# Performance work log

Hardware: AMD Instinct MI355X
Metric: run time of the kernel (lower is better)

Reference implementation:

```python
import jax, jax.numpy as jnp
import numpy as np

N, D, K, H = 16384, 2048, 8, 8
HD = D // H
LN_EPS = 1e-5


def setup_inputs() -> dict:
    key = jax.random.key(0)
    ks = jax.random.split(key, 12)
    w = lambda k: jax.random.normal(k, (D, D), dtype=jnp.float32) * 0.02
    return {
        "hidden": jax.random.normal(ks[0], (N, D), dtype=jnp.float32),
        "memory": jax.random.normal(ks[1], (K, D), dtype=jnp.float32) * 0.02,
        "w_read_q": w(ks[2]), "w_read_k": w(ks[3]), "w_read_v": w(ks[4]),
        "w_read_out": w(ks[5]),
        "w_write_q": w(ks[6]), "w_write_k": w(ks[7]), "w_write_v": w(ks[8]),
        "ln_gamma": jnp.ones((D,), dtype=jnp.float32),
        "ln_beta": jnp.zeros((D,), dtype=jnp.float32),
        "gate": jnp.full((1,), -3.0, dtype=jnp.float32),
        "write_gate": jnp.full((1,), -2.0, dtype=jnp.float32),
    }


def _layernorm(x, gamma, beta):
    mu = jnp.mean(x, axis=-1, keepdims=True)
    var = jnp.mean(jnp.square(x - mu), axis=-1, keepdims=True)
    return (x - mu) * jax.lax.rsqrt(var + LN_EPS) * gamma + beta


def reference(hidden, memory, w_read_q, w_read_k, w_read_v, w_read_out,
              w_write_q, w_write_k, w_write_v, ln_gamma, ln_beta, gate, write_gate):
    # --- read: cross-attention from tokens (queries) to memory slots (keys/values) ---
    q = (hidden @ w_read_q.T).reshape(N, H, HD)   # [N,H,hd]
    k = (memory @ w_read_k.T).reshape(K, H, HD)   # [K,H,hd]
    v = (memory @ w_read_v.T).reshape(K, H, HD)
    scores = jnp.einsum("nhd,khd->hnk", q, k) / np.sqrt(HD).astype(np.float32)
    attn = jax.nn.softmax(scores, axis=-1)        # [H,N,K]
    read_out = jnp.einsum("hnk,khd->nhd", attn, v).reshape(N, D)
    cross_info = _layernorm(read_out, ln_gamma, ln_beta) @ w_read_out.T
    g = jax.nn.sigmoid(gate[0])
    result = hidden + g * cross_info              # [N,D]
    # --- write: memory slots (queries) attend over all tokens, gated EMA update ---
    wq = memory @ w_write_q.T                     # [K,D]
    wk = hidden @ w_write_k.T                     # [N,D]
    wv = hidden @ w_write_v.T                     # [N,D]
    wattn = jax.nn.softmax(wq @ wk.T / np.sqrt(D).astype(np.float32), axis=-1)  # [K,N]
    new_info = wattn @ wv                         # [K,D]
    wg = jax.nn.sigmoid(write_gate[0])
    new_memory = (1.0 - wg) * memory + wg * new_info
    return result, new_memory
```

## Files before the change

kernel.cpp:

```cpp
#include <hip/hip_runtime.h>
#include <hip/hip_bf16.h>
#include <stdint.h>

static constexpr int N_ = 16384;
static constexpr int D_ = 2048;
static constexpr float SCALE_R = 1.0f / 16.0f;
static constexpr float SCALE_W = 0.02209708691207961f;

typedef __bf16 bf16x8 __attribute__((ext_vector_type(8)));
typedef float f32x4 __attribute__((ext_vector_type(4)));

__device__ __forceinline__ unsigned short f2bf(float f) {
  unsigned int u = __float_as_uint(f);
  unsigned int r = (u + 0x7fff + ((u >> 16) & 1)) >> 16;
  return (unsigned short)r;
}

__device__ __forceinline__ void lds_load16(void* lds, const void* g) {
  __builtin_amdgcn_global_load_lds(
      (const __attribute__((address_space(1))) uint32_t*)(uintptr_t)g,
      (__attribute__((address_space(3))) uint32_t*)(uint32_t)(uintptr_t)lds,
      16, 0, 0);
}

__global__ __launch_bounds__(256) void k_kvwq(
    const float* __restrict__ mem, const float* __restrict__ wrk,
    const float* __restrict__ wrv, const float* __restrict__ wwq,
    float* __restrict__ kbuf, float* __restrict__ vbuf, float* __restrict__ wqbuf) {
  int gw = (blockIdx.x * 256 + threadIdx.x) >> 6;
  int lane = threadIdx.x & 63;
  int which = gw >> 11;
  int j = gw & 2047;
  const float* W = which == 0 ? wrk : (which == 1 ? wrv : wwq);
  float* O = which == 0 ? kbuf : (which == 1 ? vbuf : wqbuf);
  const f32x4* Wrow = (const f32x4*)(W + (size_t)j * D_);
  const f32x4* M4 = (const f32x4*)mem;
  float acc[8];
#pragma unroll
  for (int kk = 0; kk < 8; ++kk) acc[kk] = 0.f;
#pragma unroll
  for (int t = 0; t < 8; ++t) {
    f32x4 w4 = Wrow[lane + 64 * t];
#pragma unroll
    for (int kk = 0; kk < 8; ++kk) {
      f32x4 m4 = M4[kk * 512 + lane + 64 * t];
      acc[kk] += w4[0] * m4[0] + w4[1] * m4[1] + w4[2] * m4[2] + w4[3] * m4[3];
    }
  }
#pragma unroll
  for (int off = 1; off < 64; off <<= 1)
#pragma unroll
    for (int kk = 0; kk < 8; ++kk) acc[kk] += __shfl_xor(acc[kk], off, 64);
  if (lane == 0) {
#pragma unroll
    for (int kk = 0; kk < 8; ++kk) O[kk * D_ + j] = acc[kk];
  }
}

__global__ __launch_bounds__(256) void k_pr(
    const float* __restrict__ wrq, const float* __restrict__ wwk,
    const float* __restrict__ kbuf, const float* __restrict__ wqbuf,
    float* __restrict__ PRT) {
  int b = blockIdx.x;
  int tid = threadIdx.x;
  int half = b & 1;
  int sub = (b >> 1) & 7;
  int ic = (b >> 4) & 7;
  int i = ic * 256 + tid;
  bool isP = b < 128;
  const float* W = isP ? wrq : wwk;
  const float* V = isP ? kbuf : wqbuf;
  float scale = isP ? SCALE_R : SCALE_W;
  int rowbase = isP ? sub * 8 : 64;
  float acc[8];
#pragma unroll
  for (int kk = 0; kk < 8; ++kk) acc[kk] = 0.f;
  for (int jj = half * 128; jj < half * 128 + 128; ++jj) {
    int j = sub * 256 + jj;
    float wv = W[(size_t)j * D_ + i];
#pragma unroll
    for (int kk = 0; kk < 8; ++kk) acc[kk] += wv * V[kk * D_ + j];
  }
#pragma unroll
  for (int kk = 0; kk < 8; ++kk)
    atomicAdd(&PRT[(rowbase + kk) * D_ + i], acc[kk] * scale);
}

__global__ __launch_bounds__(256) void k_prep(const float* __restrict__ wro,
                                              const float* __restrict__ gamma,
                                              const float* __restrict__ beta,
                                              unsigned short* __restrict__ wp,
                                              float* __restrict__ c1, float* __restrict__ c2) {
  __shared__ float red1[4], red2[4];
  int j = blockIdx.x;
  int tid = threadIdx.x;
  int d = tid * 8;
  const float* src = wro + (size_t)j * D_ + d;
  f32x4 a = *(const f32x4*)src, b = *(const f32x4*)(src + 4);
  f32x4 g0 = *(const f32x4*)(gamma + d), g1 = *(const f32x4*)(gamma + d + 4);
  f32x4 b0 = *(const f32x4*)(beta + d), b1 = *(const f32x4*)(beta + d + 4);
  ushort4 o0, o1;
  o0.x = f2bf(a[0] * g0[0]); o0.y = f2bf(a[1] * g0[1]);
  o0.z = f2bf(a[2] * g0[2]); o0.w = f2bf(a[3] * g0[3]);
  o1.x = f2bf(b[0] * g1[0]); o1.y = f2bf(b[1] * g1[1]);
  o1.z = f2bf(b[2] * g1[2]); o1.w = f2bf(b[3] * g1[3]);
  unsigned short* dst = wp + (size_t)j * D_ + d;
  *(ushort4*)dst = o0;
  *(ushort4*)(dst + 4) = o1;
  float s1 = a[0] * g0[0] + a[1] * g0[1] + a[2] * g0[2] + a[3] * g0[3] +
             b[0] * g1[0] + b[1] * g1[1] + b[2] * g1[2] + b[3] * g1[3];
  float s2 = a[0] * b0[0] + a[1] * b0[1] + a[2] * b0[2] + a[3] * b0[3] +
             b[0] * b1[0] + b[1] * b1[1] + b[2] * b1[2] + b[3] * b1[3];
#pragma unroll
  for (int off = 1; off < 64; off <<= 1) {
    s1 += __shfl_xor(s1, off, 64);
    s2 += __shfl_xor(s2, off, 64);
  }
  int wave = tid >> 6, lane = tid & 63;
  if (lane == 0) { red1[wave] = s1; red2[wave] = s2; }
  __syncthreads();
  if (tid == 0) {
    c1[j] = red1[0] + red1[1] + red1[2] + red1[3];
    c2[j] = red2[0] + red2[1] + red2[2] + red2[3];
  }
}

__global__ __launch_bounds__(256) void k_main(
    const float* __restrict__ hidden, const float* __restrict__ PRT,
    const float* __restrict__ vbuf,
    unsigned short* __restrict__ Xhat, float* __restrict__ mu_out,
    float* __restrict__ rstd_out,
    float* __restrict__ upart, float* __restrict__ Zpart) {
  __shared__ unsigned short Ah[2][64 * 64];
  __shared__ unsigned short Bh[2][80 * 64];
  __shared__ unsigned short attnL[64 * 64];
  __shared__ float e8lds[64][8];
  const int tid = threadIdx.x;
  const int row0 = blockIdx.x * 64;
  const int wave = tid >> 6, lane = tid & 63;
  const int fl = lane & 15, fk = lane >> 4;
  const int ar = tid >> 2, acg = tid & 3;

  f32x4 sA0[4], sB0[5], sA1[4], sB1[5];

  auto loadAB = [&](f32x4* a, f32x4* b, int t) {
    const float* srcA = hidden + (size_t)(row0 + ar) * D_ + t * 64 + acg * 16;
#pragma unroll
    for (int q = 0; q < 4; ++q) a[q] = *(const f32x4*)(srcA + q * 4);
#pragma unroll
    for (int p = 0; p < 5; ++p) {
      int e = p * 256 + tid;
      int rB = e >> 4, c4 = e & 15;
      b[p] = *(const f32x4*)(PRT + (size_t)rB * D_ + t * 64 + c4 * 4);
    }
  };
  auto writeAB = [&](int buf, f32x4* a, f32x4* b) {
#pragma unroll
    for (int hh = 0; hh < 2; ++hh) {
      f32x4 x = a[hh * 2], y = a[hh * 2 + 1];
      ushort4 o0 = {f2bf(x[0]), f2bf(x[1]), f2bf(x[2]), f2bf(x[3])};
      ushort4 o1 = {f2bf(y[0]), f2bf(y[1]), f2bf(y[2]), f2bf(y[3])};
      int idx = (ar * 64 + acg * 16 + hh * 8) ^ ((ar & 7) << 3);
      *(ushort4*)&Ah[buf][idx] = o0;
      *(ushort4*)&Ah[buf][idx + 4] = o1;
    }
#pragma unroll
    for (int p = 0; p < 5; ++p) {
      int e = p * 256 + tid;
      int rB = e >> 4, c4 = e & 15;
      ushort4 o = {f2bf(b[p][0]), f2bf(b[p][1]), f2bf(b[p][2]), f2bf(b[p][3])};
      int idx = (rB * 64 + c4 * 4) ^ ((rB & 7) << 3);
      *(ushort4*)&Bh[buf][idx] = o;
    }
  };

  f32x4 acc[5];
#pragma unroll
  for (int n = 0; n < 5; ++n) acc[n] = (f32x4){0.f, 0.f, 0.f, 0.f};

  auto compute = [&](int buf) {
#pragma unroll
    for (int kk = 0; kk < 2; ++kk) {
      int klo = kk * 32 + fk * 8;
      bf16x8 af = *(const bf16x8*)&Ah[buf][((wave * 16 + fl) * 64 + klo) ^ ((fl & 7) << 3)];
#pragma unroll
      for (int n = 0; n < 5; ++n) {
        bf16x8 bf = *(const bf16x8*)&Bh[buf][((n * 16 + fl) * 64 + klo) ^ ((fl & 7) << 3)];
        acc[n] = __builtin_amdgcn_mfma_f32_16x16x32_bf16(af, bf, acc[n], 0, 0, 0);
      }
    }
  };

  loadAB(sA0, sB0, 0);
  loadAB(sA1, sB1, 1);
  for (int t = 0; t < 32; t += 2) {
    writeAB(0, sA0, sB0);
    if (t + 2 < 32) loadAB(sA0, sB0, t + 2);
    __syncthreads();
    compute(0);
    writeAB(1, sA1, sB1);
    if (t + 3 < 32) loadAB(sA1, sB1, t + 3);
    __syncthreads();
    compute(1);
  }

#pragma unroll
  for (int r = 0; r < 4; ++r) {
    int rowl = wave * 16 + fk * 4 + r;
#pragma unroll
    for (int n = 0; n < 4; ++n) {
      float sv = acc[n][r];
      float m = sv;
      m = fmaxf(m, __shfl_xor(m, 1, 64));
      m = fmaxf(m, __shfl_xor(m, 2, 64));
      m = fmaxf(m, __shfl_xor(m, 4, 64));
      float e = __expf(sv - m);
      float ssum = e;
      ssum += __shfl_xor(ssum, 1, 64);
      ssum += __shfl_xor(ssum, 2, 64);
      ssum += __shfl_xor(ssum, 4, 64);
      attnL[rowl * 64 + n * 16 + fl] = f2bf(e / ssum);
    }
    if (fl < 8) e8lds[rowl][fl] = __expf(acc[4][r]);
  }
  __syncthreads();

  float ssum[16], ssq[16];
#pragma unroll
  for (int rw = 0; rw < 16; ++rw) { ssum[rw] = 0.f; ssq[rw] = 0.f; }
#pragma unroll
  for (int c = 0; c < 8; ++c) {
    int d0 = c * 256 + lane * 4;
    f32x4 vv[8];
#pragma unroll
    for (int kk = 0; kk < 8; ++kk) vv[kk] = *(const f32x4*)(vbuf + kk * D_ + d0);
#pragma unroll
    for (int rw = 0; rw < 16; ++rw) {
      bf16x8 at = *(const bf16x8*)&attnL[(wave * 16 + rw) * 64 + c * 8];
      f32x4 ro = (float)at[0] * vv[0] + (float)at[1] * vv[1] +
                 (float)at[2] * vv[2] + (float)at[3] * vv[3] +
                 (float)at[4] * vv[4] + (float)at[5] * vv[5] +
                 (float)at[6] * vv[6] + (float)at[7] * vv[7];
      ssum[rw] += ro[0] + ro[1] + ro[2] + ro[3];
      ssq[rw] += ro[0] * ro[0] + ro[1] * ro[1] + ro[2] * ro[2] + ro[3] * ro[3];
      ushort4 o = {f2bf(ro[0]), f2bf(ro[1]), f2bf(ro[2]), f2bf(ro[3])};
      *(ushort4*)(Xhat + (size_t)(row0 + wave * 16 + rw) * D_ + d0) = o;
    }
  }
  float muv = 0.f, rstdv = 0.f;
#pragma unroll
  for (int rw = 0; rw < 16; ++rw) {
    float s = ssum[rw], q = ssq[rw];
#pragma unroll
    for (int off = 1; off < 64; off <<= 1) {
      s += __shfl_xor(s, off, 64);
      q += __shfl_xor(q, off, 64);
    }
    float m = s * (1.f / 2048.f);
    float var = q * (1.f / 2048.f) - m * m;
    float rs = rsqrtf(var + 1e-5f);
    if (lane == rw) { muv = m; rstdv = rs; }
  }
  if (lane < 16) {
    mu_out[row0 + wave * 16 + lane] = muv;
    rstd_out[row0 + wave * 16 + lane] = rstdv;
  }
  __syncthreads();

  for (int dt = 0; dt < 2; ++dt) {
    int d0 = wave * 512 + dt * 256 + lane * 4;
    f32x4 ua[8];
#pragma unroll
    for (int kk = 0; kk < 8; ++kk) ua[kk] = (f32x4){0.f, 0.f, 0.f, 0.f};
    for (int r8 = 0; r8 < 64; r8 += 8) {
      f32x4 hv[8];
#pragma unroll
      for (int q = 0; q < 8; ++q)
        hv[q] = *(const f32x4*)(hidden + (size_t)(row0 + r8 + q) * D_ + d0);
#pragma unroll
      for (int q = 0; q < 8; ++q) {
        f32x4 e0 = *(const f32x4*)&e8lds[r8 + q][0];
        f32x4 e1 = *(const f32x4*)&e8lds[r8 + q][4];
        ua[0] += e0[0] * hv[q]; ua[1] += e0[1] * hv[q];
        ua[2] += e0[2] * hv[q]; ua[3] += e0[3] * hv[q];
        ua[4] += e1[0] * hv[q]; ua[5] += e1[1] * hv[q];
        ua[6] += e1[2] * hv[q]; ua[7] += e1[3] * hv[q];
      }
    }
#pragma unroll
    for (int kk = 0; kk < 8; ++kk)
      *(f32x4*)(upart + ((size_t)blockIdx.x * 8 + kk) * D_ + d0) = ua[kk];
  }
  if (tid < 8) {
    float z = 0.f;
    for (int r = 0; r < 64; ++r) z += e8lds[r][tid];
    Zpart[blockIdx.x * 8 + tid] = z;
  }
}

__global__ __launch_bounds__(256) void k_ured(const float* __restrict__ upart,
                                              const float* __restrict__ Zpart,
                                              float* __restrict__ tbuf) {
  int g = blockIdx.x * 256 + threadIdx.x;
  int kk = g >> 11, d = g & 2047;
  float z = 0.f;
  for (int b = 0; b < 256; ++b) z += Zpart[b * 8 + kk];
  float u = 0.f;
  for (int b = 0; b < 256; ++b) u += upart[((size_t)b * 8 + kk) * 2048 + d];
  tbuf[g] = u / z;
}

__global__ __launch_bounds__(256) void k_newmem(
    const float* __restrict__ tbuf, const float* __restrict__ wwv,
    const float* __restrict__ mem, const float* __restrict__ wgate,
    float* __restrict__ out_mem) {
  int j = (blockIdx.x * 256 + threadIdx.x) >> 6;
  int lane = threadIdx.x & 63;
  const f32x4* Wrow = (const f32x4*)(wwv + (size_t)j * D_);
  const f32x4* T4 = (const f32x4*)tbuf;
  float acc[8];
#pragma unroll
  for (int kk = 0; kk < 8; ++kk) acc[kk] = 0.f;
#pragma unroll
  for (int t = 0; t < 8; ++t) {
    f32x4 w4 = Wrow[lane + 64 * t];
#pragma unroll
    for (int kk = 0; kk < 8; ++kk) {
      f32x4 t4 = T4[kk * 512 + lane + 64 * t];
      acc[kk] += w4[0] * t4[0] + w4[1] * t4[1] + w4[2] * t4[2] + w4[3] * t4[3];
    }
  }
#pragma unroll
  for (int off = 1; off < 64; off <<= 1)
#pragma unroll
    for (int kk = 0; kk < 8; ++kk) acc[kk] += __shfl_xor(acc[kk], off, 64);
  if (lane == 0) {
    float wg = 1.f / (1.f + __expf(-wgate[0]));
#pragma unroll
    for (int kk = 0; kk < 8; ++kk)
      out_mem[kk * D_ + j] = (1.f - wg) * mem[kk * D_ + j] + wg * acc[kk];
  }
}

__global__ __launch_bounds__(256) void k_gemm(
    const unsigned short* __restrict__ A,
    const unsigned short* __restrict__ B,
    const float* __restrict__ hidden, const float* __restrict__ gate,
    const float* __restrict__ mu, const float* __restrict__ rstd,
    const float* __restrict__ c1, const float* __restrict__ c2,
    float* __restrict__ out) {
  __shared__ unsigned short As[2][128 * 64];
  __shared__ unsigned short Bs[2][128 * 64];
  const int tid = threadIdx.x;
  const int bm = blockIdx.x >> 4, bn = blockIdx.x & 15;
  const int row0 = bm * 128, col0 = bn * 128;
  const int wave = tid >> 6, lane = tid & 63;
  const int wr = wave >> 1, wc = wave & 1;
  const int fl = lane & 15, fk = lane >> 4;
  const int srow = tid >> 3;
  const int scol_l = (tid & 7) * 8;
  const int scol_g = ((tid & 7) ^ (srow & 7)) * 8;

  f32x4 acc[4][4];
#pragma unroll
  for (int m = 0; m < 4; ++m)
#pragma unroll
    for (int n = 0; n < 4; ++n) acc[m][n] = (f32x4){0.f, 0.f, 0.f, 0.f};

  auto stage = [&](int buf, int kt) {
    const int k0 = kt * 64;
#pragma unroll
    for (int p = 0; p < 4; ++p) {
      int r = srow + p * 32;
      lds_load16(&As[buf][r * 64 + scol_l], A + (size_t)(row0 + r) * D_ + k0 + scol_g);
      lds_load16(&Bs[buf][r * 64 + scol_l], B + (size_t)(col0 + r) * D_ + k0 + scol_g);
    }
  };

  stage(0, 0);
  for (int kt = 0; kt < 32; ++kt) {
    __syncthreads();
    if (kt + 1 < 32) stage((kt + 1) & 1, kt + 1);
    const int cb = kt & 1;
#pragma unroll
    for (int kkk = 0; kkk < 2; ++kkk) {
      const int gsw = ((kkk * 4 + fk) ^ (fl & 7)) * 8;
      bf16x8 af[4], bfr[4];
#pragma unroll
      for (int m = 0; m < 4; ++m)
        af[m] = *(const bf16x8*)&As[cb][(wr * 64 + m * 16 + fl) * 64 + gsw];
#pragma unroll
      for (int n = 0; n < 4; ++n)
        bfr[n] = *(const bf16x8*)&Bs[cb][(wc * 64 + n * 16 + fl) * 64 + gsw];
#pragma unroll
      for (int m = 0; m < 4; ++m)
#pragma unroll
        for (int n = 0; n < 4; ++n)
          acc[m][n] = __builtin_amdgcn_mfma_f32_16x16x32_bf16(af[m], bfr[n], acc[m][n], 0, 0, 0);
    }
  }
  float g = 1.f / (1.f + __expf(-gate[0]));
  int cols[4];
  float C1v[4], C2v[4];
#pragma unroll
  for (int n = 0; n < 4; ++n) {
    cols[n] = col0 + wc * 64 + n * 16 + fl;
    C1v[n] = c1[cols[n]] * g;
    C2v[n] = c2[cols[n]] * g;
  }
#pragma unroll
  for (int m = 0; m < 4; ++m)
#pragma unroll
    for (int r = 0; r < 4; ++r) {
      int row = row0 + wr * 64 + m * 16 + fk * 4 + r;
      float RS = rstd[row], MU = mu[row];
      const float* hrow = hidden + (size_t)row * D_;
      float* orow = out + (size_t)row * D_;
#pragma unroll
      for (int n = 0; n < 4; ++n)
        orow[cols[n]] = hrow[cols[n]] + g * RS * acc[m][n][r] - RS * MU * C1v[n] + C2v[n];
    }
}

extern "C" void kernel_launch(void* const* d_in, const int* in_sizes, int n_in,
                              void* d_out, int out_size, void* d_ws, size_t ws_size,
                              hipStream_t stream) {
  const float* hidden = (const float*)d_in[0];
  const float* mem    = (const float*)d_in[1];
  const float* wrq = (const float*)d_in[2];
  const float* wrk = (const float*)d_in[3];
  const float* wrv = (const float*)d_in[4];
  const float* wro = (const float*)d_in[5];
  const float* wwq = (const float*)d_in[6];
  const float* wwk = (const float*)d_in[7];
  const float* wwv = (const float*)d_in[8];
  const float* gamma = (const float*)d_in[9];
  const float* beta  = (const float*)d_in[10];
  const float* gate  = (const float*)d_in[11];
  const float* wgate = (const float*)d_in[12];
  float* out = (float*)d_out;

  char* ws = (char*)d_ws;
  float* kbuf  = (float*)(ws);
  float* vbuf  = (float*)(ws + (64 << 10));
  float* wqbuf = (float*)(ws + (128 << 10));
  float* PRT   = (float*)(ws + (192 << 10));
  float* tbuf  = (float*)(ws + (832 << 10));
  float* Zpart = (float*)(ws + (896 << 10));
  float* c1    = (float*)(ws + (904 << 10));
  float* c2    = (float*)(ws + (912 << 10));
  float* upart = (float*)(ws + (960ull << 10));
  unsigned short* Wp   = (unsigned short*)(ws + (960ull << 10) + (16ull << 20));
  unsigned short* Xhat = (unsigned short*)(ws + (960ull << 10) + (24ull << 20));
  float* mu   = kbuf;
  float* rstd = wqbuf;

  hipMemsetAsync(PRT, 0, 80 * 2048 * sizeof(float), stream);
  k_prep<<<2048, 256, 0, stream>>>(wro, gamma, beta, Wp, c1, c2);
  k_kvwq<<<1536, 256, 0, stream>>>(mem, wrk, wrv, wwq, kbuf, vbuf, wqbuf);
  k_pr<<<256, 256, 0, stream>>>(wrq, wwk, kbuf, wqbuf, PRT);
  k_main<<<256, 256, 0, stream>>>(hidden, PRT, vbuf, Xhat, mu, rstd, upart, Zpart);
  k_ured<<<64, 256, 0, stream>>>(upart, Zpart, tbuf);
  k_newmem<<<512, 256, 0, stream>>>(tbuf, wwv, mem, wgate, out + (size_t)N_ * D_);
  k_gemm<<<2048, 256, 0, stream>>>(Xhat, Wp, hidden, gate, mu, rstd, c1, c2, out);
}
```

Before: 343.2 us.

## Pre-convert PRT to bf16, stage via LDS DMA, widen small reduction kernels

A new small kernel converts the projected PRT matrix to bf16 once. k_main then streams it into shared memory with asynchronous global_load_lds copies, pre-swizzled, instead of loading fp32 into registers and converting per tile in every block. k_pr now uses twice as many blocks, each covering a shorter j range, and k_ured splits its 256-way sum across four waves with a shared-memory combine. Together these aim to raise parallelism in the small kernels and cut redundant conversion and register pressure in the main loop, at the cost of one extra launch and extra workspace.

```diff
diff --git a/kernel.cpp b/kernel.cpp
--- a/kernel.cpp
+++ b/kernel.cpp
@@ -63,11 +63,12 @@
     float* __restrict__ PRT) {
   int b = blockIdx.x;
   int tid = threadIdx.x;
-  int half = b & 1;
-  int sub = (b >> 1) & 7;
-  int ic = (b >> 4) & 7;
+  bool isP = b < 256;
+  int bb = isP ? b : b - 256;
+  int q = bb & 3;
+  int sub = (bb >> 2) & 7;
+  int ic = bb >> 5;
   int i = ic * 256 + tid;
-  bool isP = b < 128;
   const float* W = isP ? wrq : wwk;
   const float* V = isP ? kbuf : wqbuf;
   float scale = isP ? SCALE_R : SCALE_W;
@@ -75,8 +76,10 @@
   float acc[8];
 #pragma unroll
   for (int kk = 0; kk < 8; ++kk) acc[kk] = 0.f;
-  for (int jj = half * 128; jj < half * 128 + 128; ++jj) {
-    int j = sub * 256 + jj;
+  int j0 = sub * 256 + q * 64;
+#pragma unroll 4
+  for (int jj = 0; jj < 64; ++jj) {
+    int j = j0 + jj;
     float wv = W[(size_t)j * D_ + i];
 #pragma unroll
     for (int kk = 0; kk < 8; ++kk) acc[kk] += wv * V[kk * D_ + j];
@@ -84,6 +87,14 @@
 #pragma unroll
   for (int kk = 0; kk < 8; ++kk)
     atomicAdd(&PRT[(rowbase + kk) * D_ + i], acc[kk] * scale);
+}
+
+__global__ __launch_bounds__(256) void k_prtb(const float* __restrict__ PRT,
+                                              unsigned short* __restrict__ PRTb) {
+  int i = (blockIdx.x * 256 + threadIdx.x) * 4;
+  f32x4 v = *(const f32x4*)(PRT + i);
+  ushort4 o = {f2bf(v[0]), f2bf(v[1]), f2bf(v[2]), f2bf(v[3])};
+  *(ushort4*)(PRTb + i) = o;
 }
 
 __global__ __launch_bounds__(256) void k_prep(const float* __restrict__ wro,
@@ -126,7 +137,7 @@
 }
 
 __global__ __launch_bounds__(256) void k_main(
-    const float* __restrict__ hidden, const float* __restrict__ PRT,
+    const float* __restrict__ hidden, const unsigned short* __restrict__ PRTb,
     const float* __restrict__ vbuf,
     unsigned short* __restrict__ Xhat, float* __restrict__ mu_out,
     float* __restrict__ rstd_out,
@@ -141,20 +152,14 @@
   const int fl = lane & 15, fk = lane >> 4;
   const int ar = tid >> 2, acg = tid & 3;
 
-  f32x4 sA0[4], sB0[5], sA1[4], sB1[5];
-
-  auto loadAB = [&](f32x4* a, f32x4* b, int t) {
+  f32x4 sA0[4], sA1[4];
+
+  auto loadA = [&](f32x4* a, int t) {
     const float* srcA = hidden + (size_t)(row0 + ar) * D_ + t * 64 + acg * 16;
 #pragma unroll
     for (int q = 0; q < 4; ++q) a[q] = *(const f32x4*)(srcA + q * 4);
-#pragma unroll
-    for (int p = 0; p < 5; ++p) {
-      int e = p * 256 + tid;
-      int rB = e >> 4, c4 = e & 15;
-      b[p] = *(const f32x4*)(PRT + (size_t)rB * D_ + t * 64 + c4 * 4);
-    }
   };
-  auto writeAB = [&](int buf, f32x4* a, f32x4* b) {
+  auto writeA = [&](int buf, f32x4* a) {
 #pragma unroll
     for (int hh = 0; hh < 2; ++hh) {
       f32x4 x = a[hh * 2], y = a[hh * 2 + 1];
@@ -164,13 +169,20 @@
       *(ushort4*)&Ah[buf][idx] = o0;
       *(ushort4*)&Ah[buf][idx + 4] = o1;
     }
-#pragma unroll
-    for (int p = 0; p < 5; ++p) {
-      int e = p * 256 + tid;
-      int rB = e >> 4, c4 = e & 15;
-      ushort4 o = {f2bf(b[p][0]), f2bf(b[p][1]), f2bf(b[p][2]), f2bf(b[p][3])};
-      int idx = (rB * 64 + c4 * 4) ^ ((rB & 7) << 3);
-      *(ushort4*)&Bh[buf][idx] = o;
+  };
+  auto stageB = [&](int buf, int kt) {
+#pragma unroll
+    for (int s = 0; s < 2; ++s) {
+      int e = s * 256 + tid;
+      int rB = e >> 3, gl = e & 7, gs = gl ^ (rB & 7);
+      lds_load16(&Bh[buf][rB * 64 + gl * 8],
+                 PRTb + (size_t)rB * D_ + kt * 64 + gs * 8);
+    }
+    if (tid < 128) {
+      int e = 512 + tid;
+      int rB = e >> 3, gl = e & 7, gs = gl ^ (rB & 7);
+      lds_load16(&Bh[buf][rB * 64 + gl * 8],
+                 PRTb + (size_t)rB * D_ + kt * 64 + gs * 8);
     }
   };
 
@@ -191,16 +203,19 @@
     }
   };
 
-  loadAB(sA0, sB0, 0);
-  loadAB(sA1, sB1, 1);
+  loadA(sA0, 0);
+  loadA(sA1, 1);
+  stageB(0, 0);
   for (int t = 0; t < 32; t += 2) {
-    writeAB(0, sA0, sB0);
-    if (t + 2 < 32) loadAB(sA0, sB0, t + 2);
+    writeA(0, sA0);
+    if (t + 2 < 32) loadA(sA0, t + 2);
     __syncthreads();
+    stageB(1, t + 1);
     compute(0);
-    writeAB(1, sA1, sB1);
-    if (t + 3 < 32) loadAB(sA1, sB1, t + 3);
+    writeA(1, sA1);
+    if (t + 3 < 32) loadA(sA1, t + 3);
     __syncthreads();
+    if (t + 2 < 32) stageB(0, t + 2);
     compute(1);
   }
 
@@ -301,13 +316,24 @@
 __global__ __launch_bounds__(256) void k_ured(const float* __restrict__ upart,
                                               const float* __restrict__ Zpart,
                                               float* __restrict__ tbuf) {
-  int g = blockIdx.x * 256 + threadIdx.x;
-  int kk = g >> 11, d = g & 2047;
-  float z = 0.f;
-  for (int b = 0; b < 256; ++b) z += Zpart[b * 8 + kk];
-  float u = 0.f;
-  for (int b = 0; b < 256; ++b) u += upart[((size_t)b * 8 + kk) * 2048 + d];
-  tbuf[g] = u / z;
+  __shared__ float us[256], zs[256];
+  int tid = threadIdx.x;
+  int q = tid >> 6;
+  int o = blockIdx.x * 64 + (tid & 63);
+  int kk = o >> 11, d = o & 2047;
+  float z = 0.f, u = 0.f;
+#pragma unroll 4
+  for (int b = q * 64; b < q * 64 + 64; ++b) {
+    z += Zpart[b * 8 + kk];
+    u += upart[((size_t)b * 8 + kk) * 2048 + d];
+  }
+  us[tid] = u; zs[tid] = z;
+  __syncthreads();
+  if (q == 0) {
+    u += us[tid + 64] + us[tid + 128] + us[tid + 192];
+    z += zs[tid + 64] + zs[tid + 128] + zs[tid + 192];
+    tbuf[o] = u / z;
+  }
 }
 
 __global__ __launch_bounds__(256) void k_newmem(
@@ -449,18 +475,20 @@
   float* Zpart = (float*)(ws + (896 << 10));
   float* c1    = (float*)(ws + (904 << 10));
   float* c2    = (float*)(ws + (912 << 10));
-  float* upart = (float*)(ws + (960ull << 10));
-  unsigned short* Wp   = (unsigned short*)(ws + (960ull << 10) + (16ull << 20));
-  unsigned short* Xhat = (unsigned short*)(ws + (960ull << 10) + (24ull << 20));
+  unsigned short* PRTb = (unsigned short*)(ws + (960 << 10));
+  float* upart = (float*)(ws + (1536ull << 10));
+  unsigned short* Wp   = (unsigned short*)(ws + (1536ull << 10) + (16ull << 20));
+  unsigned short* Xhat = (unsigned short*)(ws + (1536ull << 10) + (24ull << 20));
   float* mu   = kbuf;
   float* rstd = wqbuf;
 
   hipMemsetAsync(PRT, 0, 80 * 2048 * sizeof(float), stream);
   k_prep<<<2048, 256, 0, stream>>>(wro, gamma, beta, Wp, c1, c2);
   k_kvwq<<<1536, 256, 0, stream>>>(mem, wrk, wrv, wwq, kbuf, vbuf, wqbuf);
-  k_pr<<<256, 256, 0, stream>>>(wrq, wwk, kbuf, wqbuf, PRT);
-  k_main<<<256, 256, 0, stream>>>(hidden, PRT, vbuf, Xhat, mu, rstd, upart, Zpart);
-  k_ured<<<64, 256, 0, stream>>>(upart, Zpart, tbuf);
+  k_pr<<<512, 256, 0, stream>>>(wrq, wwk, kbuf, wqbuf, PRT);
+  k_prtb<<<160, 256, 0, stream>>>(PRT, PRTb);
+  k_main<<<256, 256, 0, stream>>>(hidden, PRTb, vbuf, Xhat, mu, rstd, upart, Zpart);
+  k_ured<<<256, 256, 0, stream>>>(upart, Zpart, tbuf);
   k_newmem<<<512, 256, 0, stream>>>(tbuf, wwv, mem, wgate, out + (size_t)N_ * D_);
   k_gemm<<<2048, 256, 0, stream>>>(Xhat, Wp, hidden, gate, mu, rstd, c1, c2, out);
 }
```

New measurement: 333.7 us. 2.8% less time.
